# Kernel tuning notes

Hardware: AMD Instinct MI355X
Metric: run time of the kernel (lower is better)

Reference implementation:

```python
import jax, jax.numpy as jnp
import numpy as np

BN_EPS = 1e-5


def setup_inputs() -> dict:
    key = jax.random.key(0)
    ks = jax.random.split(key, 4)
    B, C, H, W = 4, 256, 64, 64
    Ck, Cv = 64, 256
    x = jax.random.normal(ks[0], (B, C, H, W), dtype=jnp.float32)
    Wk = jax.random.normal(ks[1], (Ck, C), dtype=jnp.float32) * (1.0 / np.sqrt(C))
    bk = jax.random.normal(ks[2], (Ck,), dtype=jnp.float32) * 0.02
    Wv = jax.random.normal(ks[3], (Cv, C), dtype=jnp.float32) * (1.0 / np.sqrt(C))
    bv = jnp.zeros((Cv,), dtype=jnp.float32)
    return {
        "x": x,
        "Wk": Wk,
        "bk": bk,
        "bn_gamma": jnp.ones((Ck,), dtype=jnp.float32),
        "bn_beta": jnp.zeros((Ck,), dtype=jnp.float32),
        "bn_mean": jnp.zeros((Ck,), dtype=jnp.float32),
        "bn_var": jnp.ones((Ck,), dtype=jnp.float32),
        "Wv": Wv,
        "bv": bv,
    }


def reference(x, Wk, bk, bn_gamma, bn_beta, bn_mean, bn_var, Wv, bv):
    B, C, H, W = x.shape
    HW = H * W
    # 1x1 conv == channel matmul; f_query = f_key (shared weights), so Q == K
    k = jnp.einsum("bchw,kc->bkhw", x, Wk) + bk[None, :, None, None]
    # BatchNorm2d (inference mode: running stats)
    inv = bn_gamma * jax.lax.rsqrt(bn_var + BN_EPS)
    k = k * inv[None, :, None, None] + (bn_beta - bn_mean * inv)[None, :, None, None]
    k = k.reshape(B, -1, HW)                      # [B, Ck, HW]
    v = (jnp.einsum("bchw,kc->bkhw", x, Wv) + bv[None, :, None, None]).reshape(B, -1, HW)  # [B, Cv, HW]
    # energy[b,i,j] = sum_c Q[b,c,i] * K[b,c,j]  (no scaling, as in source)
    energy = jnp.einsum("bci,bcj->bij", k, k)     # [B, HW, HW]
    attn = jax.nn.softmax(energy, axis=-1)
    # out[b,c,i] = sum_j V[b,c,j] * attn[i,j]
    out = jnp.einsum("bcj,bij->bci", v, attn)
    return out.reshape(B, -1, H, W)
```

## Files before the change

### kernel.cpp

```cpp
#include <hip/hip_runtime.h>
#include <math.h>

#define BN_EPS 1e-5f

constexpr int B  = 4;
constexpr int C  = 256;
constexpr int HW = 4096;
constexpr int CK = 64;
constexpr int CV = 256;
constexpr int CO = 320;
constexpr int CHG = 2;

typedef short bf16x8 __attribute__((ext_vector_type(8)));
typedef float f32x4  __attribute__((ext_vector_type(4)));
typedef unsigned uint32x4 __attribute__((ext_vector_type(4)));

__device__ __forceinline__ ushort f2bf(float f) {
    unsigned u = __float_as_uint(f);
    u += 0x7FFFu + ((u >> 16) & 1u);
    return (ushort)(u >> 16);
}

__device__ __forceinline__ unsigned cvtpk_bf16(float lo, float hi) {
    unsigned r;
    asm("v_cvt_pk_bf16_f32 %0, %1, %2" : "=v"(r) : "v"(lo), "v"(hi));
    return r;
}

__device__ __forceinline__ int swzk(int r) {
    return (((r & 3) | ((((r >> 2) ^ (r >> 3)) & 1) << 2)) << 4);
}
__device__ __forceinline__ int swzv(int r) { return (r & 7) << 4; }

__device__ __forceinline__ void gload_lds16(const void* g, void* l) {
    __builtin_amdgcn_global_load_lds(
        (const __attribute__((address_space(1))) unsigned*)g,
        (__attribute__((address_space(3))) unsigned*)l, 16, 0, 0);
}

__global__ __launch_bounds__(256) void wprep(
    const float* __restrict__ Wk, const float* __restrict__ bk,
    const float* __restrict__ gamma, const float* __restrict__ beta,
    const float* __restrict__ mean,  const float* __restrict__ var,
    const float* __restrict__ Wv, const float* __restrict__ bv,
    ushort* __restrict__ Wq, float* __restrict__ bq, unsigned* __restrict__ Mx)
{
    const int co = blockIdx.x;
    const int c  = threadIdx.x;
    if (co < B && c == 0) Mx[co] = 0u;
    float w;
    if (co < CK) {
        float inv = gamma[co] * rsqrtf(var[co] + BN_EPS);
        w = Wk[co * C + c] * inv;
        if (c == 0) bq[co] = bk[co] * inv + (beta[co] - mean[co] * inv);
    } else {
        w = Wv[(co - CK) * C + c];
        if (c == 0) bq[co] = bv[co - CK];
    }
    const int wv  = co / 80, rem = co % 80;
    const int mi  = rem / 16, colw = rem % 16;
    const int ks  = c >> 5, qw = (c >> 3) & 3, e = c & 7;
    Wq[((((((wv * 8 + ks) * 5 + mi) * 4 + qw) * 16 + colw)) << 3) + e] = f2bf(w);
}

__global__ __launch_bounds__(256) void kv_gemm(
    const float* __restrict__ x, const ushort* __restrict__ Wq,
    const float* __restrict__ bq,
    ushort* __restrict__ Kbuf, ushort* __restrict__ Vbuf,
    float* __restrict__ mb, unsigned* __restrict__ Mx)
{
    __shared__ __align__(16) ushort xt[32][C + 8];

    const int t    = threadIdx.x;
    const int lane = t & 63;
    const int wv   = t >> 6;
    const int q    = lane >> 4;
    const int col  = lane & 15;
    const int hw0  = blockIdx.x * 32;
    const int b    = blockIdx.y;

    const float* xb = x + (size_t)b * C * HW;

    {
        const int cq  = (t >> 5) * 4;
        const int hwo = t & 31;
#pragma unroll
        for (int pass = 0; pass < 8; pass++) {
            const int c0 = pass * 32;
            float a0 = xb[(size_t)(c0 + cq + 0) * HW + hw0 + hwo];
            float a1 = xb[(size_t)(c0 + cq + 1) * HW + hw0 + hwo];
            float a2 = xb[(size_t)(c0 + cq + 2) * HW + hw0 + hwo];
            float a3 = xb[(size_t)(c0 + cq + 3) * HW + hw0 + hwo];
            ushort4 u = make_ushort4(f2bf(a0), f2bf(a1), f2bf(a2), f2bf(a3));
            *(ushort4*)&xt[hwo][c0 + cq] = u;
        }
    }
    __syncthreads();

    f32x4 acc[5][2];
#pragma unroll
    for (int mi = 0; mi < 5; mi++)
#pragma unroll
        for (int nt = 0; nt < 2; nt++)
            acc[mi][nt] = (f32x4){0.f, 0.f, 0.f, 0.f};

#pragma unroll
    for (int ks = 0; ks < 8; ks++) {
        bf16x8 av[5], bvv[2];
#pragma unroll
        for (int mi = 0; mi < 5; mi++)
            av[mi] = *(const bf16x8*)(Wq + ((size_t)((wv * 8 + ks) * 5 + mi) << 9) + lane * 8);
#pragma unroll
        for (int nt = 0; nt < 2; nt++)
            bvv[nt] = *(const bf16x8*)&xt[nt * 16 + col][ks * 32 + q * 8];
#pragma unroll
        for (int mi = 0; mi < 5; mi++)
#pragma unroll
            for (int nt = 0; nt < 2; nt++)
                acc[mi][nt] = __builtin_amdgcn_mfma_f32_16x16x32_bf16(bvv[nt], av[mi], acc[mi][nt], 0, 0, 0);
    }

    float ssq[2][4] = {{0.f,0.f,0.f,0.f},{0.f,0.f,0.f,0.f}};
#pragma unroll
    for (int mi = 0; mi < 5; mi++) {
        const int cot = wv * 80 + mi * 16;
        const float bi = bq[cot + col];
#pragma unroll
        for (int nt = 0; nt < 2; nt++) {
            const int hwr = hw0 + nt * 16 + q * 4;
            float v0 = acc[mi][nt][0] + bi;
            float v1 = acc[mi][nt][1] + bi;
            float v2 = acc[mi][nt][2] + bi;
            float v3 = acc[mi][nt][3] + bi;
            if (cot < CK) {
                const int ck = cot + col;
                Kbuf[((size_t)b * HW + hwr + 0) * CK + ck] = f2bf(v0);
                Kbuf[((size_t)b * HW + hwr + 1) * CK + ck] = f2bf(v1);
                Kbuf[((size_t)b * HW + hwr + 2) * CK + ck] = f2bf(v2);
                Kbuf[((size_t)b * HW + hwr + 3) * CK + ck] = f2bf(v3);
                ssq[nt][0] += v0 * v0; ssq[nt][1] += v1 * v1;
                ssq[nt][2] += v2 * v2; ssq[nt][3] += v3 * v3;
            } else {
                const int cv = cot - CK + col;
                ushort4 vv = make_ushort4(f2bf(v0), f2bf(v1), f2bf(v2), f2bf(v3));
                *(ushort4*)&Vbuf[((size_t)b * CV + cv) * HW + hwr] = vv;
            }
        }
    }

    if (wv == 0) {
        float mxn = 0.f;
#pragma unroll
        for (int nt = 0; nt < 2; nt++) {
#pragma unroll
            for (int off = 1; off <= 8; off <<= 1)
#pragma unroll
                for (int r = 0; r < 4; r++)
                    ssq[nt][r] += __shfl_xor(ssq[nt][r], off, 64);
            float4 nr = make_float4(sqrtf(ssq[nt][0]), sqrtf(ssq[nt][1]),
                                    sqrtf(ssq[nt][2]), sqrtf(ssq[nt][3]));
            if (col == 0)
                *(float4*)&mb[(size_t)b * HW + hw0 + nt * 16 + q * 4] = nr;
            mxn = fmaxf(mxn, fmaxf(fmaxf(nr.x, nr.y), fmaxf(nr.z, nr.w)));
        }
#pragma unroll
        for (int off = 1; off <= 32; off <<= 1)
            mxn = fmaxf(mxn, __shfl_xor(mxn, off, 64));
        if (t == 0) atomicMax(Mx + b, __float_as_uint(mxn));
    }
}

__global__ __launch_bounds__(256, 2) void attn_kernel(
    const ushort* __restrict__ Kbuf, const ushort* __restrict__ Vbuf,
    const float* __restrict__ mb, const unsigned* __restrict__ Mx,
    float* __restrict__ out)
{
    __shared__ __align__(16) ushort Kt[3][64 * 64];
    __shared__ __align__(16) ushort Vt[3][128 * 64];

    const int t    = threadIdx.x;
    const int lane = t & 63;
    const int wv   = t >> 6;
    const int q    = lane >> 4;
    const int col  = lane & 15;

    const unsigned lin = blockIdx.x + 64u * (blockIdx.y + (unsigned)CHG * blockIdx.z);
    const int xcd   = lin & 7;
    const int s_    = lin >> 3;
    const int i0g   = s_ * 64;
    const int chg   = xcd & 1;
    const int b     = xcd >> 1;

    const int iw    = wv * 16 + col;
    const int jperm = (col >> 2) * 8 + (col & 3);

    const ushort* Kb = Kbuf + (size_t)b * HW * CK;
    const ushort* Vb = Vbuf + (size_t)b * CV * HW;
    const int cbase = chg * 128;

    bf16x8 qa[2];
#pragma unroll
    for (int k = 0; k < 2; k++)
        qa[k] = *(const bf16x8*)(Kb + (size_t)(i0g + iw) * CK + k * 32 + q * 8);

    const float Mxf = __uint_as_float(Mx[b]);
    const float m_val = mb[(size_t)b * HW + i0g + iw] * Mxf;

    f32x4 Oacc[8];
#pragma unroll
    for (int mt = 0; mt < 8; mt++)
        Oacc[mt] = (f32x4){0.f, 0.f, 0.f, 0.f};

    float l_acc = 0.f;
    const f32x4 zf = (f32x4){0.f, 0.f, 0.f, 0.f};

#define STAGE(BUF, JN)                                                         \
    {                                                                          \
        const int jn_s = (JN);                                                 \
        _Pragma("unroll")                                                      \
        for (int p = 0; p < 2; p++) {                                          \
            int off = (wv * 2 + p) * 1024 + lane * 16;                         \
            int r = off >> 7, cb = off & 127;                                  \
            const char* g = (const char*)Kb + (size_t)(jn_s + r) * 128         \
                            + (cb ^ swzk(r));                                  \
            gload_lds16(g, (char*)&Kt[BUF][0] + off);                          \
        }                                                                      \
        _Pragma("unroll")                                                      \
        for (int p = 0; p < 4; p++) {                                          \
            int off = (wv * 4 + p) * 1024 + lane * 16;                         \
            int r = off >> 7, cb = off & 127;                                  \
            const char* g = (const char*)Vb                                    \
                            + ((size_t)(cbase + r) * HW + jn_s) * 2            \
                            + (cb ^ swzv(r));                                  \
            gload_lds16(g, (char*)&Vt[BUF][0] + off);                          \
        }                                                                      \
    }

    STAGE(0, 0);
    STAGE(1, 64);

    int cur = 0;
    for (int j0 = 0; j0 < HW; j0 += 64) {
        asm volatile("s_waitcnt vmcnt(6)" ::: "memory");
        __builtin_amdgcn_s_barrier();
        __builtin_amdgcn_sched_barrier(0);

        const int nb = (cur + 2) % 3;
        STAGE(nb, (j0 + 128) & (HW - 1));

        const char* KtB = (const char*)&Kt[cur][0];
        const char* VtB = (const char*)&Vt[cur][0];

        f32x4 S[4];
        __builtin_amdgcn_s_setprio(1);
#pragma unroll
        for (int nt = 0; nt < 4; nt++) {
            const int jr = jperm + (nt >> 1) * 32 + (nt & 1) * 4;
            bf16x8 k0 = *(const bf16x8*)(KtB + jr * 128 + ((q * 16) ^ swzk(jr)));
            bf16x8 k1 = *(const bf16x8*)(KtB + jr * 128 + ((64 + q * 16) ^ swzk(jr)));
            S[nt] = __builtin_amdgcn_mfma_f32_16x16x32_bf16(k0, qa[0], zf, 0, 0, 0);
            S[nt] = __builtin_amdgcn_mfma_f32_16x16x32_bf16(k1, qa[1], S[nt], 0, 0, 0);
        }
        __builtin_amdgcn_s_setprio(0);

        float p[4][4];
#pragma unroll
        for (int nt = 0; nt < 4; nt++) {
            p[nt][0] = __expf(S[nt][0] - m_val);
            p[nt][1] = __expf(S[nt][1] - m_val);
            p[nt][2] = __expf(S[nt][2] - m_val);
            p[nt][3] = __expf(S[nt][3] - m_val);
            l_acc += (p[nt][0] + p[nt][1]) + (p[nt][2] + p[nt][3]);
        }
        uint32x4 U0, U1;
        U0[0] = cvtpk_bf16(p[0][0], p[0][1]);
        U0[1] = cvtpk_bf16(p[0][2], p[0][3]);
        U0[2] = cvtpk_bf16(p[1][0], p[1][1]);
        U0[3] = cvtpk_bf16(p[1][2], p[1][3]);
        U1[0] = cvtpk_bf16(p[2][0], p[2][1]);
        U1[1] = cvtpk_bf16(p[2][2], p[2][3]);
        U1[2] = cvtpk_bf16(p[3][0], p[3][1]);
        U1[3] = cvtpk_bf16(p[3][2], p[3][3]);
        bf16x8 w0 = __builtin_bit_cast(bf16x8, U0);
        bf16x8 w1 = __builtin_bit_cast(bf16x8, U1);

        __builtin_amdgcn_s_setprio(1);
#pragma unroll
        for (int mt = 0; mt < 8; mt++) {
            const int vr = mt * 16 + col;
            bf16x8 v0 = *(const bf16x8*)(VtB + vr * 128 + ((q * 16) ^ swzv(vr)));
            bf16x8 v1 = *(const bf16x8*)(VtB + vr * 128 + ((64 + q * 16) ^ swzv(vr)));
            Oacc[mt] = __builtin_amdgcn_mfma_f32_16x16x32_bf16(v0, w0, Oacc[mt], 0, 0, 0);
            Oacc[mt] = __builtin_amdgcn_mfma_f32_16x16x32_bf16(v1, w1, Oacc[mt], 0, 0, 0);
        }
        __builtin_amdgcn_s_setprio(0);

        cur = (cur + 1) % 3;
    }
#undef STAGE

    asm volatile("s_waitcnt vmcnt(0)" ::: "memory");

    l_acc += __shfl_xor(l_acc, 16, 64);
    l_acc += __shfl_xor(l_acc, 32, 64);
    const float inv = 1.0f / l_acc;

    float* ob = out + (size_t)b * CV * HW;
#pragma unroll
    for (int mt = 0; mt < 8; mt++)
#pragma unroll
        for (int r = 0; r < 4; r++)
            ob[(size_t)(cbase + mt * 16 + q * 4 + r) * HW + i0g + iw] = Oacc[mt][r] * inv;
}

extern "C" void kernel_launch(void* const* d_in, const int* in_sizes, int n_in,
                              void* d_out, int out_size, void* d_ws, size_t ws_size,
                              hipStream_t stream)
{
    const float* x     = (const float*)d_in[0];
    const float* Wk    = (const float*)d_in[1];
    const float* bk    = (const float*)d_in[2];
    const float* gamma = (const float*)d_in[3];
    const float* beta  = (const float*)d_in[4];
    const float* mean  = (const float*)d_in[5];
    const float* var   = (const float*)d_in[6];
    const float* Wv    = (const float*)d_in[7];
    const float* bv    = (const float*)d_in[8];
    float* out = (float*)d_out;

    ushort*   Kbuf = (ushort*)d_ws;
    ushort*   Vbuf = Kbuf + (size_t)B * HW * CK;
    ushort*   Wq   = Vbuf + (size_t)B * CV * HW;
    float*    bq   = (float*)(Wq + (size_t)CO * C);
    float*    mb   = bq + CO;
    unsigned* Mx   = (unsigned*)(mb + (size_t)B * HW);

    wprep<<<dim3(CO), 256, 0, stream>>>(Wk, bk, gamma, beta, mean, var, Wv, bv, Wq, bq, Mx);

    kv_gemm<<<dim3(HW / 32, B), 256, 0, stream>>>(x, Wq, bq, Kbuf, Vbuf, mb, Mx);

    dim3 g2(HW / 64, CHG, B);
    attn_kernel<<<g2, 256, 0, stream>>>(Kbuf, Vbuf, mb, Mx, out);
}
```

Baseline: 173.1 us.

## Software-pipeline QK^T of the next tile with softmax and PV of the current tile

Restructures the attention main loop so the QK MFMAs for the next key tile are issued before the exp/convert and PV MFMAs of the current tile, using two ping-ponged score register sets and a loop unrolled by two. This lets exp work on the VALU overlap with matrix-core work instead of running serially between the two GEMMs. In exchange, each iteration now waits for all outstanding loads (vmcnt(0)) rather than leaving one stage in flight, which weakens the global-to-LDS prefetch overlap. It also raises register pressure from the extra score buffers.

```diff
diff --git a/kernel.cpp b/kernel.cpp
--- a/kernel.cpp
+++ b/kernel.cpp
@@ -236,67 +236,72 @@
         }                                                                      \
     }
 
+#define QKCOMP(S, BUF)                                                         \
+    {                                                                          \
+        const char* KtB_ = (const char*)&Kt[BUF][0];                           \
+        __builtin_amdgcn_s_setprio(1);                                         \
+        _Pragma("unroll")                                                      \
+        for (int nt = 0; nt < 4; nt++) {                                       \
+            const int jr = jperm + (nt >> 1) * 32 + (nt & 1) * 4;              \
+            bf16x8 k0 = *(const bf16x8*)(KtB_ + jr * 128 + ((q * 16) ^ swzk(jr))); \
+            bf16x8 k1 = *(const bf16x8*)(KtB_ + jr * 128 + ((64 + q * 16) ^ swzk(jr))); \
+            S[nt] = __builtin_amdgcn_mfma_f32_16x16x32_bf16(k0, qa[0], zf, 0, 0, 0); \
+            S[nt] = __builtin_amdgcn_mfma_f32_16x16x32_bf16(k1, qa[1], S[nt], 0, 0, 0); \
+        }                                                                      \
+        __builtin_amdgcn_s_setprio(0);                                         \
+    }
+
+#define PHASE(SCUR, SNEXT, JSTG)                                               \
+    {                                                                          \
+        asm volatile("s_waitcnt vmcnt(0)" ::: "memory");                       \
+        __builtin_amdgcn_s_barrier();                                          \
+        __builtin_amdgcn_sched_barrier(0);                                     \
+        STAGE(stg, (JSTG));                                                    \
+        QKCOMP(SNEXT, nxt);                                                    \
+        uint32x4 U0_, U1_;                                                     \
+        _Pragma("unroll")                                                      \
+        for (int nt = 0; nt < 4; nt++) {                                       \
+            float p0 = __expf(SCUR[nt][0] - m_val);                            \
+            float p1 = __expf(SCUR[nt][1] - m_val);                            \
+            float p2 = __expf(SCUR[nt][2] - m_val);                            \
+            float p3 = __expf(SCUR[nt][3] - m_val);                            \
+            l_acc += (p0 + p1) + (p2 + p3);                                    \
+            unsigned lo_ = cvtpk_bf16(p0, p1), hi_ = cvtpk_bf16(p2, p3);       \
+            if (nt == 0)      { U0_[0] = lo_; U0_[1] = hi_; }                  \
+            else if (nt == 1) { U0_[2] = lo_; U0_[3] = hi_; }                  \
+            else if (nt == 2) { U1_[0] = lo_; U1_[1] = hi_; }                  \
+            else              { U1_[2] = lo_; U1_[3] = hi_; }                  \
+        }                                                                      \
+        bf16x8 w0 = __builtin_bit_cast(bf16x8, U0_);                           \
+        bf16x8 w1 = __builtin_bit_cast(bf16x8, U1_);                           \
+        const char* VtB_ = (const char*)&Vt[cur][0];                           \
+        __builtin_amdgcn_s_setprio(1);                                         \
+        _Pragma("unroll")                                                      \
+        for (int mt = 0; mt < 8; mt++) {                                       \
+            const int vr = mt * 16 + col;                                      \
+            bf16x8 v0 = *(const bf16x8*)(VtB_ + vr * 128 + ((q * 16) ^ swzv(vr))); \
+            bf16x8 v1 = *(const bf16x8*)(VtB_ + vr * 128 + ((64 + q * 16) ^ swzv(vr))); \
+            Oacc[mt] = __builtin_amdgcn_mfma_f32_16x16x32_bf16(v0, w0, Oacc[mt], 0, 0, 0); \
+            Oacc[mt] = __builtin_amdgcn_mfma_f32_16x16x32_bf16(v1, w1, Oacc[mt], 0, 0, 0); \
+        }                                                                      \
+        __builtin_amdgcn_s_setprio(0);                                         \
+        int tmp_ = cur; cur = nxt; nxt = stg; stg = tmp_;                      \
+    }
+
     STAGE(0, 0);
     STAGE(1, 64);
-
-    int cur = 0;
-    for (int j0 = 0; j0 < HW; j0 += 64) {
-        asm volatile("s_waitcnt vmcnt(6)" ::: "memory");
-        __builtin_amdgcn_s_barrier();
-        __builtin_amdgcn_sched_barrier(0);
-
-        const int nb = (cur + 2) % 3;
-        STAGE(nb, (j0 + 128) & (HW - 1));
-
-        const char* KtB = (const char*)&Kt[cur][0];
-        const char* VtB = (const char*)&Vt[cur][0];
-
-        f32x4 S[4];
-        __builtin_amdgcn_s_setprio(1);
-#pragma unroll
-        for (int nt = 0; nt < 4; nt++) {
-            const int jr = jperm + (nt >> 1) * 32 + (nt & 1) * 4;
-            bf16x8 k0 = *(const bf16x8*)(KtB + jr * 128 + ((q * 16) ^ swzk(jr)));
-            bf16x8 k1 = *(const bf16x8*)(KtB + jr * 128 + ((64 + q * 16) ^ swzk(jr)));
-            S[nt] = __builtin_amdgcn_mfma_f32_16x16x32_bf16(k0, qa[0], zf, 0, 0, 0);
-            S[nt] = __builtin_amdgcn_mfma_f32_16x16x32_bf16(k1, qa[1], S[nt], 0, 0, 0);
-        }
-        __builtin_amdgcn_s_setprio(0);
-
-        float p[4][4];
-#pragma unroll
-        for (int nt = 0; nt < 4; nt++) {
-            p[nt][0] = __expf(S[nt][0] - m_val);
-            p[nt][1] = __expf(S[nt][1] - m_val);
-            p[nt][2] = __expf(S[nt][2] - m_val);
-            p[nt][3] = __expf(S[nt][3] - m_val);
-            l_acc += (p[nt][0] + p[nt][1]) + (p[nt][2] + p[nt][3]);
-        }
-        uint32x4 U0, U1;
-        U0[0] = cvtpk_bf16(p[0][0], p[0][1]);
-        U0[1] = cvtpk_bf16(p[0][2], p[0][3]);
-        U0[2] = cvtpk_bf16(p[1][0], p[1][1]);
-        U0[3] = cvtpk_bf16(p[1][2], p[1][3]);
-        U1[0] = cvtpk_bf16(p[2][0], p[2][1]);
-        U1[1] = cvtpk_bf16(p[2][2], p[2][3]);
-        U1[2] = cvtpk_bf16(p[3][0], p[3][1]);
-        U1[3] = cvtpk_bf16(p[3][2], p[3][3]);
-        bf16x8 w0 = __builtin_bit_cast(bf16x8, U0);
-        bf16x8 w1 = __builtin_bit_cast(bf16x8, U1);
-
-        __builtin_amdgcn_s_setprio(1);
-#pragma unroll
-        for (int mt = 0; mt < 8; mt++) {
-            const int vr = mt * 16 + col;
-            bf16x8 v0 = *(const bf16x8*)(VtB + vr * 128 + ((q * 16) ^ swzv(vr)));
-            bf16x8 v1 = *(const bf16x8*)(VtB + vr * 128 + ((64 + q * 16) ^ swzv(vr)));
-            Oacc[mt] = __builtin_amdgcn_mfma_f32_16x16x32_bf16(v0, w0, Oacc[mt], 0, 0, 0);
-            Oacc[mt] = __builtin_amdgcn_mfma_f32_16x16x32_bf16(v1, w1, Oacc[mt], 0, 0, 0);
-        }
-        __builtin_amdgcn_s_setprio(0);
-
-        cur = (cur + 1) % 3;
-    }
+    int cur = 0, nxt = 1, stg = 2;
+    f32x4 Sa[4], Sb[4];
+    asm volatile("s_waitcnt vmcnt(6)" ::: "memory");
+    __builtin_amdgcn_s_barrier();
+    QKCOMP(Sa, 0);
+
+    for (int j0 = 0; j0 < HW; j0 += 128) {
+        PHASE(Sa, Sb, (j0 + 128) & (HW - 1));
+        PHASE(Sb, Sa, (j0 + 192) & (HW - 1));
+    }
+#undef PHASE
+#undef QKCOMP
 #undef STAGE
 
     asm volatile("s_waitcnt vmcnt(0)" ::: "memory");
```

Measured after the change: 175.2 us. No clear change (+1.2%).
